# Kernel tuning notes

Measured on AMD Instinct MI355X. Metric: run time of the kernel, lower is better.

## Reference

```python
import jax, jax.numpy as jnp
import numpy as np


def setup_inputs() -> dict:
    key = jax.random.key(0)
    k1, k2 = jax.random.split(key)
    B, S, D = 8, 2048, 128
    x = jax.random.normal(k1, (B, S, D), dtype=jnp.float32)
    y = jax.random.normal(k2, (B, S, D), dtype=jnp.float32)
    return {"x": x, "y": y}


def reference(x, y):
    # m1 = x @ y^T  -> [B, Sx, Sy]; unscaled dot-product attention
    m1 = jnp.einsum('bsd,btd->bst', x, y)
    n1 = jax.nn.softmax(m1, axis=-1)
    o1 = jnp.einsum('bst,btd->bsd', n1, y)   # [B, Sx, D]
    a1 = o1 * x                               # gating multiply

    # symmetric pass: m2 = y @ x^T (== m1 transposed)
    m2 = jnp.einsum('btd,bsd->bts', y, x)
    n2 = jax.nn.softmax(m2, axis=-1)
    o2 = jnp.einsum('bts,bsd->btd', n2, x)   # [B, Sy, D]
    a2 = o2 * y

    return jnp.concatenate([a1, a2], axis=-1)  # [B, S, 2D]
```

## Files before the change

### kernel.cpp

```cpp
#include <hip/hip_runtime.h>
#include <hip/hip_bf16.h>

typedef __attribute__((ext_vector_type(8))) short bf16x8;
typedef __attribute__((ext_vector_type(8))) _Float16 f16x8;
typedef __attribute__((ext_vector_type(4))) float f32x4;
typedef __attribute__((ext_vector_type(4))) unsigned int u32x4;

#define MFMA16B(a, b, c) __builtin_amdgcn_mfma_f32_16x16x32_bf16(a, b, c, 0, 0, 0)
#define MFMA16F(a, b, c) __builtin_amdgcn_mfma_f32_16x16x32_f16(a, b, c, 0, 0, 0)

static constexpr int S = 2048;
static constexpr int D = 128;
static constexpr int KT = 64;
static constexpr int NT = S / KT;

__device__ inline unsigned short f2b(float f) {
    union { float f; unsigned int u; } v; v.f = f;
    unsigned int u = v.u;
    return (unsigned short)((u + 0x7FFFu + ((u >> 16) & 1u)) >> 16);
}
__device__ inline float b2f(unsigned short h) {
    union { unsigned int u; float f; } v; v.u = ((unsigned int)h) << 16;
    return v.f;
}
__device__ inline unsigned int pack2(float a, float b) {
    return (unsigned int)f2b(a) | ((unsigned int)f2b(b) << 16);
}
__device__ inline unsigned int pkh(float a, float b) {
    union { _Float16 h; unsigned short u; } ua, ub;
    ua.h = (_Float16)a; ub.h = (_Float16)b;
    return (unsigned int)ua.u | ((unsigned int)ub.u << 16);
}

__global__ __launch_bounds__(256) void bimodal_prep(
    const float* __restrict__ X, const float* __restrict__ Y,
    unsigned short* __restrict__ WS)
{
    const int bid = blockIdx.x;
    const int t = bid & 31;
    const int b = (bid >> 5) & 7;
    const int mat = bid >> 8;
    const float* src = mat ? Y : X;
    char* kf = (char*)(WS + (size_t)(mat * 2 + 0) * (8ull * S * D)) + (size_t)(b * 32 + t) * 16384;
    char* vt = (char*)(WS + (size_t)(mat * 2 + 1) * (8ull * S * D)) + (size_t)(b * 32 + t) * 16384;

    __shared__ float ftile[64][129];
    const int tid = threadIdx.x;
    const float* tsrc = src + ((size_t)(b * S + t * 64)) * D;
#pragma unroll
    for (int it = 0; it < 8; ++it) {
        int idx = tid + it * 256;
        int row = idx >> 5, ch = idx & 31;
        float4 v = *(const float4*)(tsrc + (size_t)row * D + ch * 4);
        ftile[row][ch * 4 + 0] = v.x; ftile[row][ch * 4 + 1] = v.y;
        ftile[row][ch * 4 + 2] = v.z; ftile[row][ch * 4 + 3] = v.w;
    }
    __syncthreads();
#pragma unroll
    for (int it = 0; it < 16; ++it) {
        int w = tid + it * 256;
        int row = w >> 6, cp = w & 63;
        unsigned int d = pkh(ftile[row][2 * cp], ftile[row][2 * cp + 1]);
        int byte = row * 256 + cp * 4;
        byte ^= (row & 7) << 4;
        *(unsigned int*)(kf + byte) = d;
    }
#pragma unroll
    for (int it = 0; it < 16; ++it) {
        int w = tid + it * 256;
        int dd = w >> 5, jp = w & 31;
        unsigned int d = pkh(ftile[2 * jp][dd], ftile[2 * jp + 1][dd]);
        int byte = dd * 128 + jp * 4;
        byte ^= (dd & 7) << 4;
        *(unsigned int*)(vt + byte) = d;
    }
}

__global__ __launch_bounds__(256) void bimodal_attn_v3(
    const float* __restrict__ X, const float* __restrict__ Y,
    const unsigned short* __restrict__ WS, float* __restrict__ Out)
{
    const int orig = blockIdx.x;
    const int wg = (orig & 7) * 64 + (orig >> 3);
    const int qt = wg & 31;
    const int p  = (wg >> 5) & 1;
    const int b  = wg >> 6;

    const float* Q = p ? Y : X;
    const int kvmat = p ? 0 : 1;
    const int ocol = p * D;

    __shared__ unsigned short Ksh[KT * D];
    __shared__ unsigned short Vsh[D * KT];
    __shared__ unsigned int   Psh[4][16 * 36];

    const int tid = threadIdx.x;
    const int wv = tid >> 6;
    const int lane = tid & 63;
    const int c = lane & 15;
    const int g = lane >> 4;
    const int i0 = qt * 64 + wv * 16;

    const float* qrow = Q + ((size_t)(b * S + i0 + c)) * D;
    f16x8 qf[4];
#pragma unroll
    for (int kc = 0; kc < 4; ++kc) {
        const float* qp = qrow + kc * 32 + g * 8;
        float4 f0 = *(const float4*)qp;
        float4 f1 = *(const float4*)(qp + 4);
        f16x8 tq;
        tq[0] = (_Float16)f0.x; tq[1] = (_Float16)f0.y; tq[2] = (_Float16)f0.z; tq[3] = (_Float16)f0.w;
        tq[4] = (_Float16)f1.x; tq[5] = (_Float16)f1.y; tq[6] = (_Float16)f1.z; tq[7] = (_Float16)f1.w;
        qf[kc] = tq;
    }

    f32x4 o[8];
#pragma unroll
    for (int nb = 0; nb < 8; ++nb) o[nb] = (f32x4){0.f, 0.f, 0.f, 0.f};
    float m = -1e30f, l = 0.f;

    const char* kfb = (const char*)(WS + (size_t)(kvmat * 2 + 0) * (8ull * S * D)) + (size_t)b * (S * D * 2);
    const char* vtb = (const char*)(WS + (size_t)(kvmat * 2 + 1) * (8ull * S * D)) + (size_t)b * (S * D * 2);
    const int soff = wv * 4096 + lane * 16;

    u32x4 ka[4], va[4];
#pragma unroll
    for (int i = 0; i < 4; ++i) ka[i] = *(const u32x4*)(kfb + soff + i * 1024);
#pragma unroll
    for (int i = 0; i < 4; ++i) va[i] = *(const u32x4*)(vtb + soff + i * 1024);
#pragma unroll
    for (int i = 0; i < 4; ++i) *(u32x4*)((char*)Ksh + soff + i * 1024) = ka[i];
#pragma unroll
    for (int i = 0; i < 4; ++i) *(u32x4*)((char*)Vsh + soff + i * 1024) = va[i];
    __syncthreads();

    for (int tt = 0; tt < NT; ++tt) {
        const int tn = (tt + 1 < NT) ? tt + 1 : tt;
        {
            const char* kt = kfb + tn * 16384;
            const char* vp = vtb + tn * 16384;
#pragma unroll
            for (int i = 0; i < 4; ++i) ka[i] = *(const u32x4*)(kt + soff + i * 1024);
#pragma unroll
            for (int i = 0; i < 4; ++i) va[i] = *(const u32x4*)(vp + soff + i * 1024);
        }

        f32x4 sT[4];
        __builtin_amdgcn_s_setprio(1);
#pragma unroll
        for (int nb = 0; nb < 4; ++nb) {
            f32x4 acc = (f32x4){0.f, 0.f, 0.f, 0.f};
#pragma unroll
            for (int kc = 0; kc < 4; ++kc) {
                int byte = (nb * 16 + c) * 256 + kc * 64 + g * 16;
                byte ^= (c & 7) << 4;
                f16x8 kA = *(const f16x8*)((const char*)Ksh + byte);
                acc = MFMA16F(kA, qf[kc], acc);
            }
            sT[nb] = acc;
        }
        __builtin_amdgcn_s_setprio(0);

        float pmax = fmaxf(fmaxf(sT[0][0], sT[0][1]), fmaxf(sT[0][2], sT[0][3]));
#pragma unroll
        for (int nb = 1; nb < 4; ++nb)
            pmax = fmaxf(pmax, fmaxf(fmaxf(sT[nb][0], sT[nb][1]), fmaxf(sT[nb][2], sT[nb][3])));
        pmax = fmaxf(pmax, __shfl_xor(pmax, 16));
        pmax = fmaxf(pmax, __shfl_xor(pmax, 32));
        if (!__all(pmax - m <= 8.f)) {
            float mn = fmaxf(m, pmax);
            float alpha = __expf(m - mn);
            m = mn; l *= alpha;
#pragma unroll
            for (int nb = 0; nb < 8; ++nb) {
                o[nb][0] *= alpha; o[nb][1] *= alpha;
                o[nb][2] *= alpha; o[nb][3] *= alpha;
            }
        }
        float rs = 0.f;
        unsigned int* pr = Psh[wv] + c * 36;
#pragma unroll
        for (int nb = 0; nb < 4; ++nb) {
            float e0 = __expf(sT[nb][0] - m), e1 = __expf(sT[nb][1] - m);
            float e2 = __expf(sT[nb][2] - m), e3 = __expf(sT[nb][3] - m);
            rs += (e0 + e1) + (e2 + e3);
            uint2 w; w.x = pkh(e0, e1); w.y = pkh(e2, e3);
            *(uint2*)(pr + nb * 8 + 2 * g) = w;
        }
        rs += __shfl_xor(rs, 16);
        rs += __shfl_xor(rs, 32);
        l += rs;

        __builtin_amdgcn_wave_barrier();

        union { f16x8 v; u32x4 u; } pf0, pf1;
        pf0.u = *(const u32x4*)(Psh[wv] + c * 36 + 0 * 16 + 4 * g);
        pf1.u = *(const u32x4*)(Psh[wv] + c * 36 + 1 * 16 + 4 * g);

        __builtin_amdgcn_s_setprio(1);
#pragma unroll
        for (int nb = 0; nb < 8; ++nb) {
            int byte0 = (nb * 16 + c) * 128 + 0 * 64 + g * 16; byte0 ^= (c & 7) << 4;
            int byte1 = (nb * 16 + c) * 128 + 1 * 64 + g * 16; byte1 ^= (c & 7) << 4;
            f16x8 v0 = *(const f16x8*)((const char*)Vsh + byte0);
            f16x8 v1 = *(const f16x8*)((const char*)Vsh + byte1);
            o[nb] = MFMA16F(v0, pf0.v, o[nb]);
            o[nb] = MFMA16F(v1, pf1.v, o[nb]);
        }
        __builtin_amdgcn_s_setprio(0);

        __syncthreads();
#pragma unroll
        for (int i = 0; i < 4; ++i) *(u32x4*)((char*)Ksh + soff + i * 1024) = ka[i];
#pragma unroll
        for (int i = 0; i < 4; ++i) *(u32x4*)((char*)Vsh + soff + i * 1024) = va[i];
        __syncthreads();
    }

    const float inv = 1.f / l;
    float* outr = Out + ((size_t)(b * S + i0 + c)) * (2 * D) + ocol;
#pragma unroll
    for (int nb = 0; nb < 8; ++nb) {
        int d0 = nb * 16 + 4 * g;
        float4 qv = *(const float4*)(qrow + d0);
        float4 ov;
        ov.x = o[nb][0] * inv * qv.x;
        ov.y = o[nb][1] * inv * qv.y;
        ov.z = o[nb][2] * inv * qv.z;
        ov.w = o[nb][3] * inv * qv.w;
        *(float4*)(outr + d0) = ov;
    }
}

__global__ __launch_bounds__(256) void bimodal_attn_fb(
    const float* __restrict__ X, const float* __restrict__ Y,
    float* __restrict__ Out)
{
    const int bid = blockIdx.x;
    const int qt = bid & 31;
    const int p  = (bid >> 5) & 1;
    const int b  = bid >> 6;

    const float* Q  = p ? Y : X;
    const float* KV = p ? X : Y;
    const int ocol = p * D;

    __shared__ unsigned short Khi[KT * D];
    __shared__ unsigned short Klo[KT * D];
    __shared__ unsigned short Vt[D * KT];
    __shared__ unsigned short Psh[4][16 * 72];

    const int tid = threadIdx.x;
    const int wv = tid >> 6;
    const int lane = tid & 63;
    const int c = lane & 15;
    const int g = lane >> 4;
    const int i0 = qt * 64 + wv * 16;

    const float* qbase = Q + ((size_t)(b * S + i0 + c)) * D;
    bf16x8 qhi[4], qlo[4];
#pragma unroll
    for (int kc = 0; kc < 4; ++kc) {
        const float* qp = qbase + kc * 32 + g * 8;
        float4 f0 = *(const float4*)qp;
        float4 f1 = *(const float4*)(qp + 4);
        float fv[8] = {f0.x, f0.y, f0.z, f0.w, f1.x, f1.y, f1.z, f1.w};
        bf16x8 th, tl;
#pragma unroll
        for (int i = 0; i < 8; ++i) {
            unsigned short h = f2b(fv[i]);
            th[i] = (short)h;
            tl[i] = (short)f2b(fv[i] - b2f(h));
        }
        qhi[kc] = th; qlo[kc] = tl;
    }

    f32x4 o[8];
#pragma unroll
    for (int nb = 0; nb < 8; ++nb) { o[nb][0] = 0.f; o[nb][1] = 0.f; o[nb][2] = 0.f; o[nb][3] = 0.f; }
    float m[4], l[4];
#pragma unroll
    for (int r = 0; r < 4; ++r) { m[r] = -1e30f; l[r] = 0.f; }

    const float* kvb = KV + (size_t)b * S * D;
    unsigned short* pbuf = Psh[wv];

    for (int j0 = 0; j0 < S; j0 += KT) {
#pragma unroll
        for (int t = 0; t < 4; ++t) {
            int task = tid + t * 256;
            int jr = task >> 4, sl = task & 15;
            const float* src = kvb + (size_t)(j0 + jr) * D + sl * 8;
            float4 f0 = *(const float4*)src;
            float4 f1 = *(const float4*)(src + 4);
            float fv[8] = {f0.x, f0.y, f0.z, f0.w, f1.x, f1.y, f1.z, f1.w};
            unsigned short hv[8];
            float lv[8];
#pragma unroll
            for (int i = 0; i < 8; ++i) {
                hv[i] = f2b(fv[i]);
                lv[i] = fv[i] - b2f(hv[i]);
            }
            uint4 wh, wl;
            wh.x = (unsigned int)hv[0] | ((unsigned int)hv[1] << 16);
            wh.y = (unsigned int)hv[2] | ((unsigned int)hv[3] << 16);
            wh.z = (unsigned int)hv[4] | ((unsigned int)hv[5] << 16);
            wh.w = (unsigned int)hv[6] | ((unsigned int)hv[7] << 16);
            wl.x = pack2(lv[0], lv[1]); wl.y = pack2(lv[2], lv[3]);
            wl.z = pack2(lv[4], lv[5]); wl.w = pack2(lv[6], lv[7]);
            int byte = jr * 256 + sl * 16;
            byte ^= (jr & 7) << 4;
            *(uint4*)((char*)Khi + byte) = wh;
            *(uint4*)((char*)Klo + byte) = wl;
        }
#pragma unroll
        for (int t = 0; t < 2; ++t) {
            int task = tid + t * 256;
            int jp = task & 31, dc = task >> 5;
            const float* s0 = kvb + (size_t)(j0 + 2 * jp) * D + dc * 8;
            const float* s1 = s0 + D;
            float4 a0 = *(const float4*)s0, a1 = *(const float4*)(s0 + 4);
            float4 b0 = *(const float4*)s1, b1 = *(const float4*)(s1 + 4);
            float av[8] = {a0.x, a0.y, a0.z, a0.w, a1.x, a1.y, a1.z, a1.w};
            float bv[8] = {b0.x, b0.y, b0.z, b0.w, b1.x, b1.y, b1.z, b1.w};
#pragma unroll
            for (int i = 0; i < 8; ++i) {
                int d = dc * 8 + i;
                int byte = d * 128 + jp * 4;
                byte ^= (d & 7) << 4;
                *(unsigned int*)((char*)Vt + byte) = pack2(av[i], bv[i]);
            }
        }
        __syncthreads();

        f32x4 sF[4];
#pragma unroll
        for (int nb = 0; nb < 4; ++nb) {
            f32x4 acc; acc[0] = 0.f; acc[1] = 0.f; acc[2] = 0.f; acc[3] = 0.f;
#pragma unroll
            for (int kc = 0; kc < 4; ++kc) {
                int row = nb * 16 + c;
                int byte = row * 256 + (kc * 32 + g * 8) * 2;
                byte ^= (row & 7) << 4;
                bf16x8 kh = *(const bf16x8*)((char*)Khi + byte);
                bf16x8 kl = *(const bf16x8*)((char*)Klo + byte);
                acc = MFMA16B(qhi[kc], kh, acc);
                acc = MFMA16B(qhi[kc], kl, acc);
                acc = MFMA16B(qlo[kc], kh, acc);
            }
            sF[nb] = acc;
        }

#pragma unroll
        for (int r = 0; r < 4; ++r) {
            float v = fmaxf(fmaxf(sF[0][r], sF[1][r]), fmaxf(sF[2][r], sF[3][r]));
            v = fmaxf(v, __shfl_xor(v, 1));
            v = fmaxf(v, __shfl_xor(v, 2));
            v = fmaxf(v, __shfl_xor(v, 4));
            v = fmaxf(v, __shfl_xor(v, 8));
            float mn = fmaxf(m[r], v);
            float alpha = __expf(m[r] - mn);
            m[r] = mn;
            float rs = 0.f;
#pragma unroll
            for (int nb = 0; nb < 4; ++nb) {
                float pv = __expf(sF[nb][r] - mn);
                sF[nb][r] = pv;
                rs += pv;
            }
            rs += __shfl_xor(rs, 1);
            rs += __shfl_xor(rs, 2);
            rs += __shfl_xor(rs, 4);
            rs += __shfl_xor(rs, 8);
            l[r] = l[r] * alpha + rs;
#pragma unroll
            for (int nb = 0; nb < 8; ++nb) o[nb][r] *= alpha;
        }

#pragma unroll
        for (int nb = 0; nb < 4; ++nb)
#pragma unroll
            for (int r = 0; r < 4; ++r)
                pbuf[(g * 4 + r) * 72 + nb * 16 + c] = f2b(sF[nb][r]);

        bf16x8 pa[2];
#pragma unroll
        for (int kc = 0; kc < 2; ++kc)
            pa[kc] = *(const bf16x8*)(pbuf + c * 72 + kc * 32 + g * 8);

#pragma unroll
        for (int nb = 0; nb < 8; ++nb) {
#pragma unroll
            for (int kc = 0; kc < 2; ++kc) {
                int d = nb * 16 + c;
                int byte = d * 128 + (kc * 32 + g * 8) * 2;
                byte ^= (d & 7) << 4;
                bf16x8 vf = *(const bf16x8*)((char*)Vt + byte);
                o[nb] = MFMA16B(pa[kc], vf, o[nb]);
            }
        }
        __syncthreads();
    }

    float* outb = Out + ((size_t)(b * S + i0)) * (2 * D) + ocol;
    const float* qg = Q + (size_t)(b * S + i0) * D;
#pragma unroll
    for (int r = 0; r < 4; ++r) {
        int row = g * 4 + r;
        float inv = 1.f / l[r];
#pragma unroll
        for (int nb = 0; nb < 8; ++nb) {
            int col = nb * 16 + c;
            float qv = qg[(size_t)row * D + col];
            outb[(size_t)row * (2 * D) + col] = o[nb][r] * inv * qv;
        }
    }
}

extern "C" void kernel_launch(void* const* d_in, const int* in_sizes, int n_in,
                              void* d_out, int out_size, void* d_ws, size_t ws_size,
                              hipStream_t stream) {
    const float* x = (const float*)d_in[0];
    const float* y = (const float*)d_in[1];
    float* out = (float*)d_out;
    dim3 block(256);
    const size_t need = 4ull * 8 * S * D * 2;
    if (ws_size >= need) {
        dim3 pgrid(512);
        dim3 agrid(512);
        hipLaunchKernelGGL(bimodal_prep, pgrid, block, 0, stream, x, y, (unsigned short*)d_ws);
        hipLaunchKernelGGL(bimodal_attn_v3, agrid, block, 0, stream, x, y,
                           (const unsigned short*)d_ws, out);
    } else {
        dim3 fgrid(512);
        hipLaunchKernelGGL(bimodal_attn_fb, fgrid, block, 0, stream, x, y, out);
    }
}
```

Before: 77.27 us.

## Double-buffer K/V with direct global-to-LDS loads and keep P in registers

Replaces the register-staged K/V prefetch with global_load_lds direct copies into two ping-pong LDS buffers, so loading the next tile overlaps compute with one barrier per tile. The P-times-V matmul now uses 16x16x16 f16 MFMAs, whose B operand layout matches the softmax accumulator layout. P therefore stays in registers, and the per-wave LDS round trip for P is removed. The prep kernel rewrites the V-transpose layout to match the new operand ordering. This doubles K/V LDS use and issues twice as many smaller MFMAs for PV.

```diff
diff --git a/kernel.cpp b/kernel.cpp
--- a/kernel.cpp
+++ b/kernel.cpp
@@ -3,11 +3,12 @@
 
 typedef __attribute__((ext_vector_type(8))) short bf16x8;
 typedef __attribute__((ext_vector_type(8))) _Float16 f16x8;
+typedef __attribute__((ext_vector_type(4))) _Float16 f16x4;
 typedef __attribute__((ext_vector_type(4))) float f32x4;
-typedef __attribute__((ext_vector_type(4))) unsigned int u32x4;
 
 #define MFMA16B(a, b, c) __builtin_amdgcn_mfma_f32_16x16x32_bf16(a, b, c, 0, 0, 0)
 #define MFMA16F(a, b, c) __builtin_amdgcn_mfma_f32_16x16x32_f16(a, b, c, 0, 0, 0)
+#define MFMA16H(a, b, c) __builtin_amdgcn_mfma_f32_16x16x16f16(a, b, c, 0, 0, 0)
 
 static constexpr int S = 2048;
 static constexpr int D = 128;
@@ -30,6 +31,13 @@
     union { _Float16 h; unsigned short u; } ua, ub;
     ua.h = (_Float16)a; ub.h = (_Float16)b;
     return (unsigned int)ua.u | ((unsigned int)ub.u << 16);
+}
+
+__device__ __forceinline__ void gload16(const void* g, void* l) {
+    __builtin_amdgcn_global_load_lds(
+        (const __attribute__((address_space(1))) unsigned int*)(unsigned long long)(g),
+        (__attribute__((address_space(3))) unsigned int*)(unsigned int)(unsigned long long)(l),
+        16, 0, 0);
 }
 
 __global__ __launch_bounds__(256) void bimodal_prep(
@@ -69,14 +77,15 @@
     for (int it = 0; it < 16; ++it) {
         int w = tid + it * 256;
         int dd = w >> 5, jp = w & 31;
-        unsigned int d = pkh(ftile[2 * jp][dd], ftile[2 * jp + 1][dd]);
-        int byte = dd * 128 + jp * 4;
+        int j = 2 * jp;
+        unsigned int d = pkh(ftile[j][dd], ftile[j + 1][dd]);
+        int byte = dd * 128 + ((j >> 2) & 3) * 32 + (j >> 4) * 8 + (j & 3) * 2;
         byte ^= (dd & 7) << 4;
         *(unsigned int*)(vt + byte) = d;
     }
 }
 
-__global__ __launch_bounds__(256) void bimodal_attn_v3(
+__global__ __launch_bounds__(256) void bimodal_attn_v4(
     const float* __restrict__ X, const float* __restrict__ Y,
     const unsigned short* __restrict__ WS, float* __restrict__ Out)
 {
@@ -90,9 +99,10 @@
     const int kvmat = p ? 0 : 1;
     const int ocol = p * D;
 
-    __shared__ unsigned short Ksh[KT * D];
-    __shared__ unsigned short Vsh[D * KT];
-    __shared__ unsigned int   Psh[4][16 * 36];
+    __shared__ unsigned short KshA[KT * D];
+    __shared__ unsigned short KshB[KT * D];
+    __shared__ unsigned short VshA[D * KT];
+    __shared__ unsigned short VshB[D * KT];
 
     const int tid = threadIdx.x;
     const int wv = tid >> 6;
@@ -123,28 +133,16 @@
     const char* vtb = (const char*)(WS + (size_t)(kvmat * 2 + 1) * (8ull * S * D)) + (size_t)b * (S * D * 2);
     const int soff = wv * 4096 + lane * 16;
 
-    u32x4 ka[4], va[4];
-#pragma unroll
-    for (int i = 0; i < 4; ++i) ka[i] = *(const u32x4*)(kfb + soff + i * 1024);
-#pragma unroll
-    for (int i = 0; i < 4; ++i) va[i] = *(const u32x4*)(vtb + soff + i * 1024);
-#pragma unroll
-    for (int i = 0; i < 4; ++i) *(u32x4*)((char*)Ksh + soff + i * 1024) = ka[i];
-#pragma unroll
-    for (int i = 0; i < 4; ++i) *(u32x4*)((char*)Vsh + soff + i * 1024) = va[i];
-    __syncthreads();
-
-    for (int tt = 0; tt < NT; ++tt) {
-        const int tn = (tt + 1 < NT) ? tt + 1 : tt;
-        {
-            const char* kt = kfb + tn * 16384;
-            const char* vp = vtb + tn * 16384;
-#pragma unroll
-            for (int i = 0; i < 4; ++i) ka[i] = *(const u32x4*)(kt + soff + i * 1024);
-#pragma unroll
-            for (int i = 0; i < 4; ++i) va[i] = *(const u32x4*)(vp + soff + i * 1024);
-        }
-
+    auto stage = [&](unsigned short* Kb, unsigned short* Vb, int t) {
+        const char* kt = kfb + t * 16384;
+        const char* vp = vtb + t * 16384;
+#pragma unroll
+        for (int i = 0; i < 4; ++i) gload16(kt + soff + i * 1024, (char*)Kb + soff + i * 1024);
+#pragma unroll
+        for (int i = 0; i < 4; ++i) gload16(vp + soff + i * 1024, (char*)Vb + soff + i * 1024);
+    };
+
+    auto compute = [&](const unsigned short* Kb, const unsigned short* Vb) {
         f32x4 sT[4];
         __builtin_amdgcn_s_setprio(1);
 #pragma unroll
@@ -152,9 +150,8 @@
             f32x4 acc = (f32x4){0.f, 0.f, 0.f, 0.f};
 #pragma unroll
             for (int kc = 0; kc < 4; ++kc) {
-                int byte = (nb * 16 + c) * 256 + kc * 64 + g * 16;
-                byte ^= (c & 7) << 4;
-                f16x8 kA = *(const f16x8*)((const char*)Ksh + byte);
+                int byte = ((nb * 16 + c) * 256 + kc * 64 + g * 16) ^ ((c & 7) << 4);
+                f16x8 kA = *(const f16x8*)((const char*)Kb + byte);
                 acc = MFMA16F(kA, qf[kc], acc);
             }
             sT[nb] = acc;
@@ -178,42 +175,49 @@
             }
         }
         float rs = 0.f;
-        unsigned int* pr = Psh[wv] + c * 36;
+        f16x4 pB[4];
 #pragma unroll
         for (int nb = 0; nb < 4; ++nb) {
             float e0 = __expf(sT[nb][0] - m), e1 = __expf(sT[nb][1] - m);
             float e2 = __expf(sT[nb][2] - m), e3 = __expf(sT[nb][3] - m);
             rs += (e0 + e1) + (e2 + e3);
-            uint2 w; w.x = pkh(e0, e1); w.y = pkh(e2, e3);
-            *(uint2*)(pr + nb * 8 + 2 * g) = w;
+            f16x4 t;
+            t[0] = (_Float16)e0; t[1] = (_Float16)e1;
+            t[2] = (_Float16)e2; t[3] = (_Float16)e3;
+            pB[nb] = t;
         }
         rs += __shfl_xor(rs, 16);
         rs += __shfl_xor(rs, 32);
         l += rs;
 
-        __builtin_amdgcn_wave_barrier();
-
-        union { f16x8 v; u32x4 u; } pf0, pf1;
-        pf0.u = *(const u32x4*)(Psh[wv] + c * 36 + 0 * 16 + 4 * g);
-        pf1.u = *(const u32x4*)(Psh[wv] + c * 36 + 1 * 16 + 4 * g);
-
         __builtin_amdgcn_s_setprio(1);
 #pragma unroll
         for (int nb = 0; nb < 8; ++nb) {
-            int byte0 = (nb * 16 + c) * 128 + 0 * 64 + g * 16; byte0 ^= (c & 7) << 4;
-            int byte1 = (nb * 16 + c) * 128 + 1 * 64 + g * 16; byte1 ^= (c & 7) << 4;
-            f16x8 v0 = *(const f16x8*)((const char*)Vsh + byte0);
-            f16x8 v1 = *(const f16x8*)((const char*)Vsh + byte1);
-            o[nb] = MFMA16F(v0, pf0.v, o[nb]);
-            o[nb] = MFMA16F(v1, pf1.v, o[nb]);
+            int b0 = ((nb * 16 + c) * 128 + g * 32) ^ ((c & 7) << 4);
+            int b1 = b0 ^ 16;
+            f16x8 v01 = *(const f16x8*)((const char*)Vb + b0);
+            f16x8 v23 = *(const f16x8*)((const char*)Vb + b1);
+            f16x4 v0 = __builtin_shufflevector(v01, v01, 0, 1, 2, 3);
+            f16x4 v1 = __builtin_shufflevector(v01, v01, 4, 5, 6, 7);
+            f16x4 v2 = __builtin_shufflevector(v23, v23, 0, 1, 2, 3);
+            f16x4 v3 = __builtin_shufflevector(v23, v23, 4, 5, 6, 7);
+            o[nb] = MFMA16H(v0, pB[0], o[nb]);
+            o[nb] = MFMA16H(v1, pB[1], o[nb]);
+            o[nb] = MFMA16H(v2, pB[2], o[nb]);
+            o[nb] = MFMA16H(v3, pB[3], o[nb]);
         }
         __builtin_amdgcn_s_setprio(0);
-
+    };
+
+    stage(KshA, VshA, 0);
+    __syncthreads();
+
+    for (int tp = 0; tp < NT; tp += 2) {
+        stage(KshB, VshB, tp + 1);
+        compute(KshA, VshA);
         __syncthreads();
-#pragma unroll
-        for (int i = 0; i < 4; ++i) *(u32x4*)((char*)Ksh + soff + i * 1024) = ka[i];
-#pragma unroll
-        for (int i = 0; i < 4; ++i) *(u32x4*)((char*)Vsh + soff + i * 1024) = va[i];
+        if (tp + 2 < NT) stage(KshA, VshA, tp + 2);
+        compute(KshB, VshB);
         __syncthreads();
     }
 
@@ -429,7 +433,7 @@
         dim3 pgrid(512);
         dim3 agrid(512);
         hipLaunchKernelGGL(bimodal_prep, pgrid, block, 0, stream, x, y, (unsigned short*)d_ws);
-        hipLaunchKernelGGL(bimodal_attn_v3, agrid, block, 0, stream, x, y,
+        hipLaunchKernelGGL(bimodal_attn_v4, agrid, block, 0, stream, x, y,
                            (const unsigned short*)d_ws, out);
     } else {
         dim3 fgrid(512);
```

Result: faster. 75.42 us (-2.4%).

## Restructure attention with 32x32 MFMA, split-KV wave groups, and async LDS loads

Applied to the files above, without the earlier changes.

Replaces the 16x16x32 f16 MFMA attention kernel with a 32x32x16 variant. Each 512-thread block handles 128 queries, and its two wave groups split the KV tiles and merge their softmax states at the end. K/V tiles (now 32 rows) are double-buffered through global_load_lds direct-to-LDS copies instead of register staging. P is formed in registers with v_permlane32_swap, which removes the LDS round trip. The aim is fewer LDS operations and better MFMA efficiency, at the cost of a cross-group reduction through shared memory and half as many blocks (256).

```diff
diff --git a/kernel.cpp b/kernel.cpp
--- a/kernel.cpp
+++ b/kernel.cpp
@@ -4,15 +4,13 @@
 typedef __attribute__((ext_vector_type(8))) short bf16x8;
 typedef __attribute__((ext_vector_type(8))) _Float16 f16x8;
 typedef __attribute__((ext_vector_type(4))) float f32x4;
-typedef __attribute__((ext_vector_type(4))) unsigned int u32x4;
+typedef __attribute__((ext_vector_type(16))) float f32x16;
 
 #define MFMA16B(a, b, c) __builtin_amdgcn_mfma_f32_16x16x32_bf16(a, b, c, 0, 0, 0)
-#define MFMA16F(a, b, c) __builtin_amdgcn_mfma_f32_16x16x32_f16(a, b, c, 0, 0, 0)
+#define MFMA32F(a, b, c) __builtin_amdgcn_mfma_f32_32x32x16_f16(a, b, c, 0, 0, 0)
 
 static constexpr int S = 2048;
 static constexpr int D = 128;
-static constexpr int KT = 64;
-static constexpr int NT = S / KT;
 
 __device__ inline unsigned short f2b(float f) {
     union { float f; unsigned int u; } v; v.f = f;
@@ -32,23 +30,30 @@
     return (unsigned int)ua.u | ((unsigned int)ub.u << 16);
 }
 
-__global__ __launch_bounds__(256) void bimodal_prep(
+__device__ __forceinline__ void gload16(const void* g, void* l) {
+    __builtin_amdgcn_global_load_lds(
+        (const __attribute__((address_space(1))) unsigned int*)(unsigned long long)(g),
+        (__attribute__((address_space(3))) unsigned int*)(unsigned int)(unsigned long long)(l),
+        16, 0, 0);
+}
+
+__global__ __launch_bounds__(256) void bimodal_prep5(
     const float* __restrict__ X, const float* __restrict__ Y,
     unsigned short* __restrict__ WS)
 {
     const int bid = blockIdx.x;
-    const int t = bid & 31;
-    const int b = (bid >> 5) & 7;
-    const int mat = bid >> 8;
+    const int t = bid & 63;
+    const int b = (bid >> 6) & 7;
+    const int mat = bid >> 9;
     const float* src = mat ? Y : X;
-    char* kf = (char*)(WS + (size_t)(mat * 2 + 0) * (8ull * S * D)) + (size_t)(b * 32 + t) * 16384;
-    char* vt = (char*)(WS + (size_t)(mat * 2 + 1) * (8ull * S * D)) + (size_t)(b * 32 + t) * 16384;
-
-    __shared__ float ftile[64][129];
+    char* kf = (char*)(WS + (size_t)(mat * 2 + 0) * (8ull * S * D)) + (size_t)(b * 64 + t) * 8192;
+    char* vt = (char*)(WS + (size_t)(mat * 2 + 1) * (8ull * S * D)) + (size_t)(b * 64 + t) * 8192;
+
+    __shared__ float ftile[32][129];
     const int tid = threadIdx.x;
-    const float* tsrc = src + ((size_t)(b * S + t * 64)) * D;
-#pragma unroll
-    for (int it = 0; it < 8; ++it) {
+    const float* tsrc = src + ((size_t)(b * S + t * 32)) * D;
+#pragma unroll
+    for (int it = 0; it < 4; ++it) {
         int idx = tid + it * 256;
         int row = idx >> 5, ch = idx & 31;
         float4 v = *(const float4*)(tsrc + (size_t)row * D + ch * 4);
@@ -57,178 +62,202 @@
     }
     __syncthreads();
 #pragma unroll
-    for (int it = 0; it < 16; ++it) {
+    for (int it = 0; it < 8; ++it) {
         int w = tid + it * 256;
         int row = w >> 6, cp = w & 63;
         unsigned int d = pkh(ftile[row][2 * cp], ftile[row][2 * cp + 1]);
-        int byte = row * 256 + cp * 4;
-        byte ^= (row & 7) << 4;
+        int byte = (row * 256 + cp * 4) ^ ((row & 7) << 4);
         *(unsigned int*)(kf + byte) = d;
     }
 #pragma unroll
-    for (int it = 0; it < 16; ++it) {
+    for (int it = 0; it < 8; ++it) {
         int w = tid + it * 256;
-        int dd = w >> 5, jp = w & 31;
+        int dd = w >> 4, jp = w & 15;
         unsigned int d = pkh(ftile[2 * jp][dd], ftile[2 * jp + 1][dd]);
-        int byte = dd * 128 + jp * 4;
-        byte ^= (dd & 7) << 4;
+        int byte = (dd * 64 + jp * 4) ^ ((dd & 7) << 4);
         *(unsigned int*)(vt + byte) = d;
     }
 }
 
-__global__ __launch_bounds__(256) void bimodal_attn_v3(
+__global__ __launch_bounds__(512) void bimodal_attn_v5(
     const float* __restrict__ X, const float* __restrict__ Y,
     const unsigned short* __restrict__ WS, float* __restrict__ Out)
 {
     const int orig = blockIdx.x;
-    const int wg = (orig & 7) * 64 + (orig >> 3);
-    const int qt = wg & 31;
-    const int p  = (wg >> 5) & 1;
-    const int b  = wg >> 6;
+    const int wg = (orig & 7) * 32 + (orig >> 3);
+    const int qt = wg & 15;
+    const int p  = (wg >> 4) & 1;
+    const int b  = wg >> 5;
 
     const float* Q = p ? Y : X;
     const int kvmat = p ? 0 : 1;
     const int ocol = p * D;
 
-    __shared__ unsigned short Ksh[KT * D];
-    __shared__ unsigned short Vsh[D * KT];
-    __shared__ unsigned int   Psh[4][16 * 36];
+    __shared__ __align__(16) char smem[65536];
 
     const int tid = threadIdx.x;
     const int wv = tid >> 6;
     const int lane = tid & 63;
-    const int c = lane & 15;
-    const int g = lane >> 4;
-    const int i0 = qt * 64 + wv * 16;
-
-    const float* qrow = Q + ((size_t)(b * S + i0 + c)) * D;
-    f16x8 qf[4];
-#pragma unroll
-    for (int kc = 0; kc < 4; ++kc) {
-        const float* qp = qrow + kc * 32 + g * 8;
-        float4 f0 = *(const float4*)qp;
-        float4 f1 = *(const float4*)(qp + 4);
+    const int qp = lane & 31;
+    const int h = lane >> 5;
+    const int grp = wv >> 2;
+    const int qb = wv & 3;
+    const int i0 = qt * 128 + qb * 32;
+
+    const float* qrow = Q + ((size_t)(b * S + i0 + qp)) * D;
+    f16x8 qf[8];
+#pragma unroll
+    for (int kc = 0; kc < 8; ++kc) {
+        const float* qpp = qrow + kc * 16 + h * 8;
+        float4 f0 = *(const float4*)qpp;
+        float4 f1 = *(const float4*)(qpp + 4);
         f16x8 tq;
         tq[0] = (_Float16)f0.x; tq[1] = (_Float16)f0.y; tq[2] = (_Float16)f0.z; tq[3] = (_Float16)f0.w;
         tq[4] = (_Float16)f1.x; tq[5] = (_Float16)f1.y; tq[6] = (_Float16)f1.z; tq[7] = (_Float16)f1.w;
         qf[kc] = tq;
     }
 
-    f32x4 o[8];
-#pragma unroll
-    for (int nb = 0; nb < 8; ++nb) o[nb] = (f32x4){0.f, 0.f, 0.f, 0.f};
+    f32x16 o[4];
+#pragma unroll
+    for (int db = 0; db < 4; ++db)
+#pragma unroll
+        for (int i = 0; i < 16; ++i) o[db][i] = 0.f;
     float m = -1e30f, l = 0.f;
 
     const char* kfb = (const char*)(WS + (size_t)(kvmat * 2 + 0) * (8ull * S * D)) + (size_t)b * (S * D * 2);
     const char* vtb = (const char*)(WS + (size_t)(kvmat * 2 + 1) * (8ull * S * D)) + (size_t)b * (S * D * 2);
-    const int soff = wv * 4096 + lane * 16;
-
-    u32x4 ka[4], va[4];
-#pragma unroll
-    for (int i = 0; i < 4; ++i) ka[i] = *(const u32x4*)(kfb + soff + i * 1024);
-#pragma unroll
-    for (int i = 0; i < 4; ++i) va[i] = *(const u32x4*)(vtb + soff + i * 1024);
-#pragma unroll
-    for (int i = 0; i < 4; ++i) *(u32x4*)((char*)Ksh + soff + i * 1024) = ka[i];
-#pragma unroll
-    for (int i = 0; i < 4; ++i) *(u32x4*)((char*)Vsh + soff + i * 1024) = va[i];
+    const int gl = qb * 64 + lane;
+    char* mybase = smem + grp * 32768;
+
+    auto stage = [&](int t, int bi) {
+        char* kb = mybase + bi * 16384;
+        char* vb = kb + 8192;
+        const char* kt = kfb + t * 8192;
+        const char* vp = vtb + t * 8192;
+        gload16(kt + gl * 16, kb + gl * 16);
+        gload16(kt + 4096 + gl * 16, kb + 4096 + gl * 16);
+        gload16(vp + gl * 16, vb + gl * 16);
+        gload16(vp + 4096 + gl * 16, vb + 4096 + gl * 16);
+    };
+
+    stage(grp, 0);
     __syncthreads();
 
-    for (int tt = 0; tt < NT; ++tt) {
-        const int tn = (tt + 1 < NT) ? tt + 1 : tt;
-        {
-            const char* kt = kfb + tn * 16384;
-            const char* vp = vtb + tn * 16384;
-#pragma unroll
-            for (int i = 0; i < 4; ++i) ka[i] = *(const u32x4*)(kt + soff + i * 1024);
-#pragma unroll
-            for (int i = 0; i < 4; ++i) va[i] = *(const u32x4*)(vp + soff + i * 1024);
-        }
-
-        f32x4 sT[4];
+    for (int s = 0; s < 32; ++s) {
+        if (s < 31) stage(2 * (s + 1) + grp, (s + 1) & 1);
+        const char* kb = mybase + (s & 1) * 16384;
+        const char* vb = kb + 8192;
+
+        f32x16 sT;
+#pragma unroll
+        for (int i = 0; i < 16; ++i) sT[i] = 0.f;
         __builtin_amdgcn_s_setprio(1);
 #pragma unroll
-        for (int nb = 0; nb < 4; ++nb) {
-            f32x4 acc = (f32x4){0.f, 0.f, 0.f, 0.f};
-#pragma unroll
-            for (int kc = 0; kc < 4; ++kc) {
-                int byte = (nb * 16 + c) * 256 + kc * 64 + g * 16;
-                byte ^= (c & 7) << 4;
-                f16x8 kA = *(const f16x8*)((const char*)Ksh + byte);
-                acc = MFMA16F(kA, qf[kc], acc);
-            }
-            sT[nb] = acc;
+        for (int kc = 0; kc < 8; ++kc) {
+            int byte = (qp * 256 + kc * 32 + h * 16) ^ ((qp & 7) << 4);
+            f16x8 kA = *(const f16x8*)(kb + byte);
+            sT = MFMA32F(kA, qf[kc], sT);
         }
         __builtin_amdgcn_s_setprio(0);
 
-        float pmax = fmaxf(fmaxf(sT[0][0], sT[0][1]), fmaxf(sT[0][2], sT[0][3]));
-#pragma unroll
-        for (int nb = 1; nb < 4; ++nb)
-            pmax = fmaxf(pmax, fmaxf(fmaxf(sT[nb][0], sT[nb][1]), fmaxf(sT[nb][2], sT[nb][3])));
-        pmax = fmaxf(pmax, __shfl_xor(pmax, 16));
+        float pmax = sT[0];
+#pragma unroll
+        for (int i = 1; i < 16; ++i) pmax = fmaxf(pmax, sT[i]);
         pmax = fmaxf(pmax, __shfl_xor(pmax, 32));
         if (!__all(pmax - m <= 8.f)) {
             float mn = fmaxf(m, pmax);
             float alpha = __expf(m - mn);
             m = mn; l *= alpha;
 #pragma unroll
-            for (int nb = 0; nb < 8; ++nb) {
-                o[nb][0] *= alpha; o[nb][1] *= alpha;
-                o[nb][2] *= alpha; o[nb][3] *= alpha;
-            }
+            for (int db = 0; db < 4; ++db)
+#pragma unroll
+                for (int i = 0; i < 16; ++i) o[db][i] *= alpha;
         }
         float rs = 0.f;
-        unsigned int* pr = Psh[wv] + c * 36;
-#pragma unroll
-        for (int nb = 0; nb < 4; ++nb) {
-            float e0 = __expf(sT[nb][0] - m), e1 = __expf(sT[nb][1] - m);
-            float e2 = __expf(sT[nb][2] - m), e3 = __expf(sT[nb][3] - m);
-            rs += (e0 + e1) + (e2 + e3);
-            uint2 w; w.x = pkh(e0, e1); w.y = pkh(e2, e3);
-            *(uint2*)(pr + nb * 8 + 2 * g) = w;
-        }
-        rs += __shfl_xor(rs, 16);
+#pragma unroll
+        for (int i = 0; i < 16; ++i) { sT[i] = __expf(sT[i] - m); rs += sT[i]; }
         rs += __shfl_xor(rs, 32);
         l += rs;
 
-        __builtin_amdgcn_wave_barrier();
-
-        union { f16x8 v; u32x4 u; } pf0, pf1;
-        pf0.u = *(const u32x4*)(Psh[wv] + c * 36 + 0 * 16 + 4 * g);
-        pf1.u = *(const u32x4*)(Psh[wv] + c * 36 + 1 * 16 + 4 * g);
+        unsigned w8[8];
+#pragma unroll
+        for (int t2 = 0; t2 < 4; ++t2) {
+            w8[2 * t2]     = pkh(sT[4 * t2 + 0], sT[4 * t2 + 1]);
+            w8[2 * t2 + 1] = pkh(sT[4 * t2 + 2], sT[4 * t2 + 3]);
+        }
+        union { unsigned u[4]; f16x8 v; } bf0, bf1;
+#pragma unroll
+        for (int v2 = 0; v2 < 2; ++v2) {
+            unsigned a0 = w8[v2], b0 = w8[2 + v2];
+            asm volatile("v_permlane32_swap_b32 %0, %1" : "+v"(a0), "+v"(b0));
+            bf0.u[v2] = a0; bf0.u[2 + v2] = b0;
+            unsigned a1 = w8[4 + v2], b1 = w8[6 + v2];
+            asm volatile("v_permlane32_swap_b32 %0, %1" : "+v"(a1), "+v"(b1));
+            bf1.u[v2] = a1; bf1.u[2 + v2] = b1;
+        }
 
         __builtin_amdgcn_s_setprio(1);
 #pragma unroll
-        for (int nb = 0; nb < 8; ++nb) {
-            int byte0 = (nb * 16 + c) * 128 + 0 * 64 + g * 16; byte0 ^= (c & 7) << 4;
-            int byte1 = (nb * 16 + c) * 128 + 1 * 64 + g * 16; byte1 ^= (c & 7) << 4;
-            f16x8 v0 = *(const f16x8*)((const char*)Vsh + byte0);
-            f16x8 v1 = *(const f16x8*)((const char*)Vsh + byte1);
-            o[nb] = MFMA16F(v0, pf0.v, o[nb]);
-            o[nb] = MFMA16F(v1, pf1.v, o[nb]);
+        for (int db = 0; db < 4; ++db) {
+            int rowbyte = (db * 32 + qp) * 64;
+            int x0 = (rowbyte + h * 16) ^ ((qp & 7) << 4);
+            int x1 = (rowbyte + 32 + h * 16) ^ ((qp & 7) << 4);
+            f16x8 v0 = *(const f16x8*)(vb + x0);
+            f16x8 v1 = *(const f16x8*)(vb + x1);
+            o[db] = MFMA32F(v0, bf0.v, o[db]);
+            o[db] = MFMA32F(v1, bf1.v, o[db]);
         }
         __builtin_amdgcn_s_setprio(0);
 
         __syncthreads();
-#pragma unroll
-        for (int i = 0; i < 4; ++i) *(u32x4*)((char*)Ksh + soff + i * 1024) = ka[i];
-#pragma unroll
-        for (int i = 0; i < 4; ++i) *(u32x4*)((char*)Vsh + soff + i * 1024) = va[i];
+    }
+
+    {
+        float2* mlp = (float2*)(smem + wv * 512);
+        mlp[lane] = make_float2(m, l);
+    }
+    __syncthreads();
+    float2 pml = ((float2*)(smem + (wv ^ 4) * 512))[lane];
+    float mstar = fmaxf(m, pml.x);
+    float sc = __expf(m - mstar);
+    float lstar = sc * l + __expf(pml.x - mstar) * pml.y;
+#pragma unroll
+    for (int db = 0; db < 4; ++db)
+#pragma unroll
+        for (int i = 0; i < 16; ++i) o[db][i] *= sc;
+    __syncthreads();
+
+    float* obuf = (float*)(smem + 4096) + qb * 1024 + lane * 16;
+#pragma unroll
+    for (int db = 0; db < 4; ++db) {
+        if (grp == 1) {
+#pragma unroll
+            for (int i = 0; i < 16; ++i) obuf[i] = o[db][i];
+        }
         __syncthreads();
-    }
-
-    const float inv = 1.f / l;
-    float* outr = Out + ((size_t)(b * S + i0 + c)) * (2 * D) + ocol;
-#pragma unroll
-    for (int nb = 0; nb < 8; ++nb) {
-        int d0 = nb * 16 + 4 * g;
-        float4 qv = *(const float4*)(qrow + d0);
-        float4 ov;
-        ov.x = o[nb][0] * inv * qv.x;
-        ov.y = o[nb][1] * inv * qv.y;
-        ov.z = o[nb][2] * inv * qv.z;
-        ov.w = o[nb][3] * inv * qv.w;
-        *(float4*)(outr + d0) = ov;
+        if (grp == 0) {
+#pragma unroll
+            for (int i = 0; i < 16; ++i) o[db][i] += obuf[i];
+        }
+        __syncthreads();
+    }
+
+    if (grp == 0) {
+        const float invl = 1.f / lstar;
+        float* outr = Out + ((size_t)(b * S + i0 + qp)) * (2 * D) + ocol;
+#pragma unroll
+        for (int db = 0; db < 4; ++db)
+#pragma unroll
+            for (int t2 = 0; t2 < 4; ++t2) {
+                int d0 = db * 32 + t2 * 8 + h * 4;
+                float4 qv = *(const float4*)(qrow + d0);
+                float4 ov;
+                ov.x = o[db][4 * t2 + 0] * invl * qv.x;
+                ov.y = o[db][4 * t2 + 1] * invl * qv.y;
+                ov.z = o[db][4 * t2 + 2] * invl * qv.z;
+                ov.w = o[db][4 * t2 + 3] * invl * qv.w;
+                *(float4*)(outr + d0) = ov;
+            }
     }
 }
 
@@ -245,9 +274,9 @@
     const float* KV = p ? X : Y;
     const int ocol = p * D;
 
-    __shared__ unsigned short Khi[KT * D];
-    __shared__ unsigned short Klo[KT * D];
-    __shared__ unsigned short Vt[D * KT];
+    __shared__ unsigned short Khi[64 * D];
+    __shared__ unsigned short Klo[64 * D];
+    __shared__ unsigned short Vt[D * 64];
     __shared__ unsigned short Psh[4][16 * 72];
 
     const int tid = threadIdx.x;
@@ -268,9 +297,9 @@
         bf16x8 th, tl;
 #pragma unroll
         for (int i = 0; i < 8; ++i) {
-            unsigned short h = f2b(fv[i]);
-            th[i] = (short)h;
-            tl[i] = (short)f2b(fv[i] - b2f(h));
+            unsigned short hh = f2b(fv[i]);
+            th[i] = (short)hh;
+            tl[i] = (short)f2b(fv[i] - b2f(hh));
         }
         qhi[kc] = th; qlo[kc] = tl;
     }
@@ -285,7 +314,7 @@
     const float* kvb = KV + (size_t)b * S * D;
     unsigned short* pbuf = Psh[wv];
 
-    for (int j0 = 0; j0 < S; j0 += KT) {
+    for (int j0 = 0; j0 < S; j0 += 64) {
 #pragma unroll
         for (int t = 0; t < 4; ++t) {
             int task = tid + t * 256;
@@ -308,8 +337,7 @@
             wh.w = (unsigned int)hv[6] | ((unsigned int)hv[7] << 16);
             wl.x = pack2(lv[0], lv[1]); wl.y = pack2(lv[2], lv[3]);
             wl.z = pack2(lv[4], lv[5]); wl.w = pack2(lv[6], lv[7]);
-            int byte = jr * 256 + sl * 16;
-            byte ^= (jr & 7) << 4;
+            int byte = (jr * 256 + sl * 16) ^ ((jr & 7) << 4);
             *(uint4*)((char*)Khi + byte) = wh;
             *(uint4*)((char*)Klo + byte) = wl;
         }
@@ -326,8 +354,7 @@
 #pragma unroll
             for (int i = 0; i < 8; ++i) {
                 int d = dc * 8 + i;
-                int byte = d * 128 + jp * 4;
-                byte ^= (d & 7) << 4;
+                int byte = (d * 128 + jp * 4) ^ ((d & 7) << 4);
                 *(unsigned int*)((char*)Vt + byte) = pack2(av[i], bv[i]);
             }
         }
@@ -340,8 +367,7 @@
 #pragma unroll
             for (int kc = 0; kc < 4; ++kc) {
                 int row = nb * 16 + c;
-                int byte = row * 256 + (kc * 32 + g * 8) * 2;
-                byte ^= (row & 7) << 4;
+                int byte = (row * 256 + (kc * 32 + g * 8) * 2) ^ ((row & 7) << 4);
                 bf16x8 kh = *(const bf16x8*)((char*)Khi + byte);
                 bf16x8 kl = *(const bf16x8*)((char*)Klo + byte);
                 acc = MFMA16B(qhi[kc], kh, acc);
@@ -393,8 +419,7 @@
 #pragma unroll
             for (int kc = 0; kc < 2; ++kc) {
                 int d = nb * 16 + c;
-                int byte = d * 128 + (kc * 32 + g * 8) * 2;
-                byte ^= (d & 7) << 4;
+                int byte = (d * 128 + (kc * 32 + g * 8) * 2) ^ ((d & 7) << 4);
                 bf16x8 vf = *(const bf16x8*)((char*)Vt + byte);
                 o[nb] = MFMA16B(pa[kc], vf, o[nb]);
             }
@@ -423,16 +448,13 @@
     const float* x = (const float*)d_in[0];
     const float* y = (const float*)d_in[1];
     float* out = (float*)d_out;
-    dim3 block(256);
     const size_t need = 4ull * 8 * S * D * 2;
     if (ws_size >= need) {
-        dim3 pgrid(512);
-        dim3 agrid(512);
-        hipLaunchKernelGGL(bimodal_prep, pgrid, block, 0, stream, x, y, (unsigned short*)d_ws);
-        hipLaunchKernelGGL(bimodal_attn_v3, agrid, block, 0, stream, x, y,
-                           (const unsigned short*)d_ws, out);
+        hipLaunchKernelGGL(bimodal_prep5, dim3(1024), dim3(256), 0, stream,
+                           x, y, (unsigned short*)d_ws);
+        hipLaunchKernelGGL(bimodal_attn_v5, dim3(256), dim3(512), 0, stream,
+                           x, y, (const unsigned short*)d_ws, out);
     } else {
-        dim3 fgrid(512);
-        hipLaunchKernelGGL(bimodal_attn_fb, fgrid, block, 0, stream, x, y, out);
-    }
-}
+        hipLaunchKernelGGL(bimodal_attn_fb, dim3(512), dim3(256), 0, stream, x, y, out);
+    }
+}
```

After: 66.18 us. -14.4%, faster.
